# Kernel optimization log

Measured on AMD Instinct MI355X. Metric: run time of the kernel, lower is better.

The kernel has to match this reference:

```python
import jax, jax.numpy as jnp
import numpy as np

N = 8192        # batch rows
D = 1024        # final_dim (power of 2, == init_dim so padding = 0)
STACK = 4       # nbr_stack
SIGMA = 1.0


def _hadamard(n):
    H = np.array([[1.0]], dtype=np.float32)
    while H.shape[0] < n:
        H = np.block([[H, H], [H, -H]])
    return H


def setup_inputs() -> dict:
    key = jax.random.key(0)
    x = jax.random.normal(key, (N, D), dtype=jnp.float32)
    rs = np.random.RandomState(0)
    # B: random signs (diag), shape (STACK, D)
    B = jnp.asarray(rs.choice([-1.0, 1.0], size=(STACK, D)).astype(np.float32))
    # G: gaussian diag, flattened to (STACK*D,)
    G2 = rs.randn(STACK, D).astype(np.float32)
    G = jnp.asarray(G2.reshape(STACK * D))
    # S: chi-like scaling normalized by per-stack norm of G, flattened
    G_norm = np.linalg.norm(G2, axis=1, keepdims=True)
    S2 = (np.abs(rs.randn(STACK, D)).astype(np.float32) * np.sqrt(D)) / G_norm
    S = jnp.asarray(S2.reshape(STACK * D).astype(np.float32))
    # H: dense Walsh-Hadamard matrix (D, D), +-1 entries (non-trainable constant)
    H = jnp.asarray(_hadamard(D))
    # P: per-stack permutation with stack offsets, gathered along feature axis
    P = jnp.asarray(np.concatenate([rs.permutation(D) + i * D for i in range(STACK)]).astype(np.int32))
    bias = jnp.zeros((2 * STACK * D,), dtype=jnp.float32)
    return {"x": x, "B": B, "G": G, "S": S, "bias": bias, "H": H, "P": P}


def reference(x, B, G, S, bias, H, P):
    n = x.shape[0]
    # padding = final_dim - init_dim = 0 here; pad kept for faithfulness
    xp = jnp.pad(x.reshape(-1, D), ((0, 0), (0, 0)))
    # diag B then Hadamard matmul: [n, STACK, D]
    h = xp[:, None, :] * B
    h = jnp.einsum('nsd,de->nse', h, H).reshape(n, STACK * D)
    # permutation gather, diag G
    h = h[:, P] * G
    # second Hadamard matmul
    h = jnp.einsum('nsd,de->nse', h.reshape(n, STACK, D), H).reshape(n, STACK * D)
    # scale by 1/(sigma*sqrt(D)) and diag S
    h = (1.0 / (SIGMA * np.sqrt(D))) * h * S
    # cos/sin random-feature activation
    out = np.sqrt(1.0 / D).astype(np.float32) * jnp.concatenate([jnp.cos(h), jnp.sin(h)], axis=1)
    out = out + bias
    return out
```

## Files before the change

### kernel.cpp

```cpp
#include <hip/hip_runtime.h>


#define FF_D 1024
#define FF_STACK 4
#define FF_NT 256

#define SWZF(vf, OFF) \
    __int_as_float(__builtin_amdgcn_ds_swizzle(__float_as_int(vf), (OFF)))

#define STAGE_BIT(vv, m) { \
    _Pragma("unroll") \
    for (int i_ = 0; i_ < 16; ++i_) \
        if (!(i_ & (m))) { \
            float s_ = vv[i_] + vv[i_ | (m)]; \
            float d_ = vv[i_] - vv[i_ | (m)]; \
            vv[i_] = s_; vv[i_ | (m)] = d_; \
        } \
}

#define STAGE_SWZ(vv, OFF, sgn) { \
    float p_[16]; \
    _Pragma("unroll") \
    for (int i_ = 0; i_ < 16; ++i_) p_[i_] = SWZF(vv[i_], OFF); \
    _Pragma("unroll") \
    for (int i_ = 0; i_ < 16; ++i_) vv[i_] = __builtin_fmaf(sgn, vv[i_], p_[i_]); \
}

#define STAGE_X32(vv, sgn) { \
    float p_[16]; \
    _Pragma("unroll") \
    for (int i_ = 0; i_ < 16; ++i_) p_[i_] = __shfl_xor(vv[i_], 32, 64); \
    _Pragma("unroll") \
    for (int i_ = 0; i_ < 16; ++i_) vv[i_] = __builtin_fmaf(sgn, vv[i_], p_[i_]); \
}

#define FWHT10(vv) { \
    STAGE_BIT(vv, 1) STAGE_BIT(vv, 2) STAGE_BIT(vv, 4) STAGE_BIT(vv, 8) \
    STAGE_SWZ(vv, 0x041F, sg1)   \
    STAGE_SWZ(vv, 0x081F, sg2)   \
    STAGE_SWZ(vv, 0x101F, sg4)   \
    STAGE_SWZ(vv, 0x201F, sg8)   \
    STAGE_SWZ(vv, 0x401F, sg16)  \
    STAGE_X32(vv, sg32)          \
}

__global__ __launch_bounds__(FF_NT) void fastfood_kernel(
    const float* __restrict__ x,
    const float* __restrict__ Bs,
    const float* __restrict__ G,
    const float* __restrict__ S,
    const float* __restrict__ bias,
    const int*   __restrict__ P,
    float* __restrict__ out)
{
    __shared__ float lds[FF_STACK * FF_D];
    const int lane = threadIdx.x & 63;
    const int s    = threadIdx.x >> 6;
    const int row  = blockIdx.x;
    const int sb   = s << 10;
    float* wl = lds + sb;

    const float sg1  = (lane & 1)  ? -1.0f : 1.0f;
    const float sg2  = (lane & 2)  ? -1.0f : 1.0f;
    const float sg4  = (lane & 4)  ? -1.0f : 1.0f;
    const float sg8  = (lane & 8)  ? -1.0f : 1.0f;
    const float sg16 = (lane & 16) ? -1.0f : 1.0f;
    const float sg32 = (lane & 32) ? -1.0f : 1.0f;

    const float kout = 0.03125f;
    const float karg = 0.03125f * 0.15915494309f;

    float v[16];

    #pragma unroll
    for (int q = 0; q < 4; ++q) {
        const float4 t  = *(const float4*)&x[((long long)row << 10) + (q << 8) + (lane << 2)];
        const float4 b4 = *(const float4*)&Bs[sb + (q << 8) + (lane << 2)];
        v[4*q+0] = t.x * b4.x; v[4*q+1] = t.y * b4.y;
        v[4*q+2] = t.z * b4.z; v[4*q+3] = t.w * b4.w;
    }

    FWHT10(v)

    #pragma unroll
    for (int q = 0; q < 4; ++q)
        *(float4*)&wl[(q << 8) | (lane << 2)] =
            make_float4(v[4*q], v[4*q+1], v[4*q+2], v[4*q+3]);
    __builtin_amdgcn_wave_barrier();
    #pragma unroll
    for (int q = 0; q < 4; ++q) {
        const int jb = sb + (q << 8) + (lane << 2);
        const int4   p4 = *(const int4*)&P[jb];
        const float4 g4 = *(const float4*)&G[jb];
        v[4*q+0] = wl[p4.x & (FF_D - 1)] * g4.x;
        v[4*q+1] = wl[p4.y & (FF_D - 1)] * g4.y;
        v[4*q+2] = wl[p4.z & (FF_D - 1)] * g4.z;
        v[4*q+3] = wl[p4.w & (FF_D - 1)] * g4.w;
    }

    FWHT10(v)

    const long long obase = ((long long)row << 13);
    #pragma unroll
    for (int q = 0; q < 4; ++q) {
        const int j = sb + (q << 8) + (lane << 2);
        const float4 s4  = *(const float4*)&S[j];
        const float4 bc4 = *(const float4*)&bias[j];
        const float4 bs4 = *(const float4*)&bias[FF_STACK * FF_D + j];
        float4 oc, os;
        {
            const float tr = __builtin_amdgcn_fractf(v[4*q+0] * (s4.x * karg));
            oc.x = __builtin_amdgcn_cosf(tr) * kout + bc4.x;
            os.x = __builtin_amdgcn_sinf(tr) * kout + bs4.x;
        }
        {
            const float tr = __builtin_amdgcn_fractf(v[4*q+1] * (s4.y * karg));
            oc.y = __builtin_amdgcn_cosf(tr) * kout + bc4.y;
            os.y = __builtin_amdgcn_sinf(tr) * kout + bs4.y;
        }
        {
            const float tr = __builtin_amdgcn_fractf(v[4*q+2] * (s4.z * karg));
            oc.z = __builtin_amdgcn_cosf(tr) * kout + bc4.z;
            os.z = __builtin_amdgcn_sinf(tr) * kout + bs4.z;
        }
        {
            const float tr = __builtin_amdgcn_fractf(v[4*q+3] * (s4.w * karg));
            oc.w = __builtin_amdgcn_cosf(tr) * kout + bc4.w;
            os.w = __builtin_amdgcn_sinf(tr) * kout + bs4.w;
        }
        *(float4*)&out[obase + j] = oc;
        *(float4*)&out[obase + FF_STACK * FF_D + j] = os;
    }
}

extern "C" void kernel_launch(void* const* d_in, const int* in_sizes, int n_in,
                              void* d_out, int out_size, void* d_ws, size_t ws_size,
                              hipStream_t stream) {
    const float* x    = (const float*)d_in[0];
    const float* B    = (const float*)d_in[1];
    const float* G    = (const float*)d_in[2];
    const float* S    = (const float*)d_in[3];
    const float* bias = (const float*)d_in[4];
    const int*   P    = (const int*)d_in[6];
    float* out = (float*)d_out;

    const int n_rows = in_sizes[0] / FF_D;
    fastfood_kernel<<<n_rows, FF_NT, 0, stream>>>(x, B, G, S, bias, P, out);
}
```

Measured before the change: 326.3 us.

## Process two rows per block to reuse B, P, G, S, bias loads and add ILP

Each block now handles two consecutive rows, interleaving both FWHT pipelines so swizzles and butterflies of two independent rows overlap. The per-stack constants (B, P, G, S, bias) are loaded once and shared by both rows, and the P/G loads are hoisted ahead of the LDS write. The cost is twice the register and LDS footprint per block and half as many blocks, which may lower occupancy. It assumes an even row count.

```diff
diff --git a/kernel.cpp b/kernel.cpp
--- a/kernel.cpp
+++ b/kernel.cpp
@@ -8,40 +8,58 @@
 #define SWZF(vf, OFF) \
     __int_as_float(__builtin_amdgcn_ds_swizzle(__float_as_int(vf), (OFF)))
 
-#define STAGE_BIT(vv, m) { \
+#define STAGE_BIT2(aa, bb, m) { \
     _Pragma("unroll") \
     for (int i_ = 0; i_ < 16; ++i_) \
         if (!(i_ & (m))) { \
-            float s_ = vv[i_] + vv[i_ | (m)]; \
-            float d_ = vv[i_] - vv[i_ | (m)]; \
-            vv[i_] = s_; vv[i_ | (m)] = d_; \
+            float sa_ = aa[i_] + aa[i_ | (m)]; \
+            float da_ = aa[i_] - aa[i_ | (m)]; \
+            aa[i_] = sa_; aa[i_ | (m)] = da_; \
+            float sb_ = bb[i_] + bb[i_ | (m)]; \
+            float db_ = bb[i_] - bb[i_ | (m)]; \
+            bb[i_] = sb_; bb[i_ | (m)] = db_; \
         } \
 }
 
-#define STAGE_SWZ(vv, OFF, sgn) { \
-    float p_[16]; \
+#define STAGE_SWZ2(aa, bb, OFF, sgn) { \
+    float pa_[16], pb_[16]; \
     _Pragma("unroll") \
-    for (int i_ = 0; i_ < 16; ++i_) p_[i_] = SWZF(vv[i_], OFF); \
+    for (int i_ = 0; i_ < 16; ++i_) pa_[i_] = SWZF(aa[i_], OFF); \
     _Pragma("unroll") \
-    for (int i_ = 0; i_ < 16; ++i_) vv[i_] = __builtin_fmaf(sgn, vv[i_], p_[i_]); \
+    for (int i_ = 0; i_ < 16; ++i_) pb_[i_] = SWZF(bb[i_], OFF); \
+    _Pragma("unroll") \
+    for (int i_ = 0; i_ < 16; ++i_) aa[i_] = __builtin_fmaf(sgn, aa[i_], pa_[i_]); \
+    _Pragma("unroll") \
+    for (int i_ = 0; i_ < 16; ++i_) bb[i_] = __builtin_fmaf(sgn, bb[i_], pb_[i_]); \
 }
 
-#define STAGE_X32(vv, sgn) { \
-    float p_[16]; \
+#define STAGE_X32_2(aa, bb, sgn) { \
+    float pa_[16], pb_[16]; \
     _Pragma("unroll") \
-    for (int i_ = 0; i_ < 16; ++i_) p_[i_] = __shfl_xor(vv[i_], 32, 64); \
+    for (int i_ = 0; i_ < 16; ++i_) pa_[i_] = __shfl_xor(aa[i_], 32, 64); \
     _Pragma("unroll") \
-    for (int i_ = 0; i_ < 16; ++i_) vv[i_] = __builtin_fmaf(sgn, vv[i_], p_[i_]); \
+    for (int i_ = 0; i_ < 16; ++i_) pb_[i_] = __shfl_xor(bb[i_], 32, 64); \
+    _Pragma("unroll") \
+    for (int i_ = 0; i_ < 16; ++i_) aa[i_] = __builtin_fmaf(sgn, aa[i_], pa_[i_]); \
+    _Pragma("unroll") \
+    for (int i_ = 0; i_ < 16; ++i_) bb[i_] = __builtin_fmaf(sgn, bb[i_], pb_[i_]); \
 }
 
-#define FWHT10(vv) { \
-    STAGE_BIT(vv, 1) STAGE_BIT(vv, 2) STAGE_BIT(vv, 4) STAGE_BIT(vv, 8) \
-    STAGE_SWZ(vv, 0x041F, sg1)   \
-    STAGE_SWZ(vv, 0x081F, sg2)   \
-    STAGE_SWZ(vv, 0x101F, sg4)   \
-    STAGE_SWZ(vv, 0x201F, sg8)   \
-    STAGE_SWZ(vv, 0x401F, sg16)  \
-    STAGE_X32(vv, sg32)          \
+#define FWHT10_2(aa, bb) { \
+    STAGE_BIT2(aa, bb, 1) STAGE_BIT2(aa, bb, 2) \
+    STAGE_BIT2(aa, bb, 4) STAGE_BIT2(aa, bb, 8) \
+    STAGE_SWZ2(aa, bb, 0x041F, sg1)   \
+    STAGE_SWZ2(aa, bb, 0x081F, sg2)   \
+    STAGE_SWZ2(aa, bb, 0x101F, sg4)   \
+    STAGE_SWZ2(aa, bb, 0x201F, sg8)   \
+    STAGE_SWZ2(aa, bb, 0x401F, sg16)  \
+    STAGE_X32_2(aa, bb, sg32)         \
+}
+
+#define CS1(val, sc, bc, bs, oC, oS) { \
+    const float tr_ = __builtin_amdgcn_fractf((val) * ((sc) * karg)); \
+    oC = __builtin_amdgcn_cosf(tr_) * kout + (bc); \
+    oS = __builtin_amdgcn_sinf(tr_) * kout + (bs); \
 }
 
 __global__ __launch_bounds__(FF_NT) void fastfood_kernel(
@@ -53,12 +71,13 @@
     const int*   __restrict__ P,
     float* __restrict__ out)
 {
-    __shared__ float lds[FF_STACK * FF_D];
+    __shared__ float lds[2 * FF_STACK * FF_D];
     const int lane = threadIdx.x & 63;
     const int s    = threadIdx.x >> 6;
-    const int row  = blockIdx.x;
+    const int row0 = blockIdx.x << 1;
     const int sb   = s << 10;
-    float* wl = lds + sb;
+    float* wl0 = lds + sb;
+    float* wl1 = lds + FF_STACK * FF_D + sb;
 
     const float sg1  = (lane & 1)  ? -1.0f : 1.0f;
     const float sg2  = (lane & 2)  ? -1.0f : 1.0f;
@@ -70,66 +89,73 @@
     const float kout = 0.03125f;
     const float karg = 0.03125f * 0.15915494309f;
 
-    float v[16];
+    float v0[16], v1[16];
 
+    const long long xb0 = ((long long)row0 << 10);
     #pragma unroll
     for (int q = 0; q < 4; ++q) {
-        const float4 t  = *(const float4*)&x[((long long)row << 10) + (q << 8) + (lane << 2)];
-        const float4 b4 = *(const float4*)&Bs[sb + (q << 8) + (lane << 2)];
-        v[4*q+0] = t.x * b4.x; v[4*q+1] = t.y * b4.y;
-        v[4*q+2] = t.z * b4.z; v[4*q+3] = t.w * b4.w;
+        const int eo = (q << 8) + (lane << 2);
+        const float4 t0 = *(const float4*)&x[xb0 + eo];
+        const float4 t1 = *(const float4*)&x[xb0 + FF_D + eo];
+        const float4 b4 = *(const float4*)&Bs[sb + eo];
+        v0[4*q+0] = t0.x * b4.x; v0[4*q+1] = t0.y * b4.y;
+        v0[4*q+2] = t0.z * b4.z; v0[4*q+3] = t0.w * b4.w;
+        v1[4*q+0] = t1.x * b4.x; v1[4*q+1] = t1.y * b4.y;
+        v1[4*q+2] = t1.z * b4.z; v1[4*q+3] = t1.w * b4.w;
     }
 
-    FWHT10(v)
+    FWHT10_2(v0, v1)
 
+    int4   p4[4];
+    float4 g4[4];
     #pragma unroll
-    for (int q = 0; q < 4; ++q)
-        *(float4*)&wl[(q << 8) | (lane << 2)] =
-            make_float4(v[4*q], v[4*q+1], v[4*q+2], v[4*q+3]);
+    for (int q = 0; q < 4; ++q) {
+        const int jb = sb + (q << 8) + (lane << 2);
+        p4[q] = *(const int4*)&P[jb];
+        g4[q] = *(const float4*)&G[jb];
+    }
+    #pragma unroll
+    for (int q = 0; q < 4; ++q) {
+        const int eo = (q << 8) | (lane << 2);
+        *(float4*)&wl0[eo] = make_float4(v0[4*q], v0[4*q+1], v0[4*q+2], v0[4*q+3]);
+        *(float4*)&wl1[eo] = make_float4(v1[4*q], v1[4*q+1], v1[4*q+2], v1[4*q+3]);
+    }
     __builtin_amdgcn_wave_barrier();
     #pragma unroll
     for (int q = 0; q < 4; ++q) {
-        const int jb = sb + (q << 8) + (lane << 2);
-        const int4   p4 = *(const int4*)&P[jb];
-        const float4 g4 = *(const float4*)&G[jb];
-        v[4*q+0] = wl[p4.x & (FF_D - 1)] * g4.x;
-        v[4*q+1] = wl[p4.y & (FF_D - 1)] * g4.y;
-        v[4*q+2] = wl[p4.z & (FF_D - 1)] * g4.z;
-        v[4*q+3] = wl[p4.w & (FF_D - 1)] * g4.w;
+        const int ix = p4[q].x & (FF_D - 1);
+        const int iy = p4[q].y & (FF_D - 1);
+        const int iz = p4[q].z & (FF_D - 1);
+        const int iw = p4[q].w & (FF_D - 1);
+        v0[4*q+0] = wl0[ix] * g4[q].x;  v1[4*q+0] = wl1[ix] * g4[q].x;
+        v0[4*q+1] = wl0[iy] * g4[q].y;  v1[4*q+1] = wl1[iy] * g4[q].y;
+        v0[4*q+2] = wl0[iz] * g4[q].z;  v1[4*q+2] = wl1[iz] * g4[q].z;
+        v0[4*q+3] = wl0[iw] * g4[q].w;  v1[4*q+3] = wl1[iw] * g4[q].w;
     }
 
-    FWHT10(v)
+    FWHT10_2(v0, v1)
 
-    const long long obase = ((long long)row << 13);
+    const long long ob0 = ((long long)row0 << 13);
+    const long long ob1 = ob0 + (FF_STACK * FF_D * 2);
     #pragma unroll
     for (int q = 0; q < 4; ++q) {
         const int j = sb + (q << 8) + (lane << 2);
         const float4 s4  = *(const float4*)&S[j];
         const float4 bc4 = *(const float4*)&bias[j];
         const float4 bs4 = *(const float4*)&bias[FF_STACK * FF_D + j];
-        float4 oc, os;
-        {
-            const float tr = __builtin_amdgcn_fractf(v[4*q+0] * (s4.x * karg));
-            oc.x = __builtin_amdgcn_cosf(tr) * kout + bc4.x;
-            os.x = __builtin_amdgcn_sinf(tr) * kout + bs4.x;
-        }
-        {
-            const float tr = __builtin_amdgcn_fractf(v[4*q+1] * (s4.y * karg));
-            oc.y = __builtin_amdgcn_cosf(tr) * kout + bc4.y;
-            os.y = __builtin_amdgcn_sinf(tr) * kout + bs4.y;
-        }
-        {
-            const float tr = __builtin_amdgcn_fractf(v[4*q+2] * (s4.z * karg));
-            oc.z = __builtin_amdgcn_cosf(tr) * kout + bc4.z;
-            os.z = __builtin_amdgcn_sinf(tr) * kout + bs4.z;
-        }
-        {
-            const float tr = __builtin_amdgcn_fractf(v[4*q+3] * (s4.w * karg));
-            oc.w = __builtin_amdgcn_cosf(tr) * kout + bc4.w;
-            os.w = __builtin_amdgcn_sinf(tr) * kout + bs4.w;
-        }
-        *(float4*)&out[obase + j] = oc;
-        *(float4*)&out[obase + FF_STACK * FF_D + j] = os;
+        float4 oc0, os0, oc1, os1;
+        CS1(v0[4*q+0], s4.x, bc4.x, bs4.x, oc0.x, os0.x)
+        CS1(v1[4*q+0], s4.x, bc4.x, bs4.x, oc1.x, os1.x)
+        CS1(v0[4*q+1], s4.y, bc4.y, bs4.y, oc0.y, os0.y)
+        CS1(v1[4*q+1], s4.y, bc4.y, bs4.y, oc1.y, os1.y)
+        CS1(v0[4*q+2], s4.z, bc4.z, bs4.z, oc0.z, os0.z)
+        CS1(v1[4*q+2], s4.z, bc4.z, bs4.z, oc1.z, os1.z)
+        CS1(v0[4*q+3], s4.w, bc4.w, bs4.w, oc0.w, os0.w)
+        CS1(v1[4*q+3], s4.w, bc4.w, bs4.w, oc1.w, os1.w)
+        *(float4*)&out[ob0 + j] = oc0;
+        *(float4*)&out[ob0 + FF_STACK * FF_D + j] = os0;
+        *(float4*)&out[ob1 + j] = oc1;
+        *(float4*)&out[ob1 + FF_STACK * FF_D + j] = os1;
     }
 }
 
@@ -145,5 +171,5 @@
     float* out = (float*)d_out;
 
     const int n_rows = in_sizes[0] / FF_D;
-    fastfood_kernel<<<n_rows, FF_NT, 0, stream>>>(x, B, G, S, bias, P, out);
+    fastfood_kernel<<<n_rows / 2, FF_NT, 0, stream>>>(x, B, G, S, bias, P, out);
 }
```

Result: faster. 305.3 us (-6.4%).

## Split each Hadamard stack across two waves and use DPP for lane butterflies

Applied to the files above, without the earlier changes.

Each 1024-point transform is now split across two waves, with each thread holding 8 values instead of 16. The top butterfly stage is folded into the loads by combining own and partner halves of the input, so each wave reads both halves. The grid doubles to two blocks per row. Several ds_swizzle lane exchanges are replaced with DPP quad_perm and row_ror moves, and launch_bounds asks for 6 blocks per CU. The aim is lower register pressure and more parallelism. The cost is twice the global loads of x, B, P and G, plus a block-wide __syncthreads in place of the wave barrier.

```diff
diff --git a/kernel.cpp b/kernel.cpp
--- a/kernel.cpp
+++ b/kernel.cpp
@@ -8,9 +8,13 @@
 #define SWZF(vf, OFF) \
     __int_as_float(__builtin_amdgcn_ds_swizzle(__float_as_int(vf), (OFF)))
 
-#define STAGE_BIT(vv, m) { \
+#define DPPF(vf, CTRL) \
+    __int_as_float(__builtin_amdgcn_update_dpp( \
+        __float_as_int(vf), __float_as_int(vf), (CTRL), 0xF, 0xF, false))
+
+#define STAGE_BIT8(vv, m) { \
     _Pragma("unroll") \
-    for (int i_ = 0; i_ < 16; ++i_) \
+    for (int i_ = 0; i_ < 8; ++i_) \
         if (!(i_ & (m))) { \
             float s_ = vv[i_] + vv[i_ | (m)]; \
             float d_ = vv[i_] - vv[i_ | (m)]; \
@@ -18,33 +22,47 @@
         } \
 }
 
-#define STAGE_SWZ(vv, OFF, sgn) { \
-    float p_[16]; \
+#define STAGE_DPP8(vv, CTRL, sgn) { \
+    float p_[8]; \
     _Pragma("unroll") \
-    for (int i_ = 0; i_ < 16; ++i_) p_[i_] = SWZF(vv[i_], OFF); \
+    for (int i_ = 0; i_ < 8; ++i_) p_[i_] = DPPF(vv[i_], CTRL); \
     _Pragma("unroll") \
-    for (int i_ = 0; i_ < 16; ++i_) vv[i_] = __builtin_fmaf(sgn, vv[i_], p_[i_]); \
+    for (int i_ = 0; i_ < 8; ++i_) vv[i_] = __builtin_fmaf(sgn, vv[i_], p_[i_]); \
 }
 
-#define STAGE_X32(vv, sgn) { \
-    float p_[16]; \
+#define STAGE_SWZ8(vv, OFF, sgn) { \
+    float p_[8]; \
     _Pragma("unroll") \
-    for (int i_ = 0; i_ < 16; ++i_) p_[i_] = __shfl_xor(vv[i_], 32, 64); \
+    for (int i_ = 0; i_ < 8; ++i_) p_[i_] = SWZF(vv[i_], OFF); \
     _Pragma("unroll") \
-    for (int i_ = 0; i_ < 16; ++i_) vv[i_] = __builtin_fmaf(sgn, vv[i_], p_[i_]); \
+    for (int i_ = 0; i_ < 8; ++i_) vv[i_] = __builtin_fmaf(sgn, vv[i_], p_[i_]); \
 }
 
-#define FWHT10(vv) { \
-    STAGE_BIT(vv, 1) STAGE_BIT(vv, 2) STAGE_BIT(vv, 4) STAGE_BIT(vv, 8) \
-    STAGE_SWZ(vv, 0x041F, sg1)   \
-    STAGE_SWZ(vv, 0x081F, sg2)   \
-    STAGE_SWZ(vv, 0x101F, sg4)   \
-    STAGE_SWZ(vv, 0x201F, sg8)   \
-    STAGE_SWZ(vv, 0x401F, sg16)  \
-    STAGE_X32(vv, sg32)          \
+#define STAGE_X32_8(vv, sgn) { \
+    float p_[8]; \
+    _Pragma("unroll") \
+    for (int i_ = 0; i_ < 8; ++i_) p_[i_] = __shfl_xor(vv[i_], 32, 64); \
+    _Pragma("unroll") \
+    for (int i_ = 0; i_ < 8; ++i_) vv[i_] = __builtin_fmaf(sgn, vv[i_], p_[i_]); \
 }
 
-__global__ __launch_bounds__(FF_NT) void fastfood_kernel(
+#define FWHT9(vv) { \
+    STAGE_BIT8(vv, 1) STAGE_BIT8(vv, 2) STAGE_BIT8(vv, 4) \
+    STAGE_DPP8(vv, 0xB1, sgL1)     \
+    STAGE_DPP8(vv, 0x4E, sgL2)     \
+    STAGE_SWZ8(vv, 0x101F, sgL4)   \
+    STAGE_DPP8(vv, 0x128, sgL8)    \
+    STAGE_SWZ8(vv, 0x401F, sgL16)  \
+    STAGE_X32_8(vv, sgL32)         \
+}
+
+#define CS1(val, sc, bc, bs, oC, oS) { \
+    const float tr_ = __builtin_amdgcn_fractf((val) * ((sc) * karg)); \
+    oC = __builtin_amdgcn_cosf(tr_) * kout + (bc); \
+    oS = __builtin_amdgcn_sinf(tr_) * kout + (bs); \
+}
+
+__global__ __launch_bounds__(FF_NT, 6) void fastfood_kernel(
     const float* __restrict__ x,
     const float* __restrict__ Bs,
     const float* __restrict__ G,
@@ -53,83 +71,93 @@
     const int*   __restrict__ P,
     float* __restrict__ out)
 {
-    __shared__ float lds[FF_STACK * FF_D];
-    const int lane = threadIdx.x & 63;
-    const int s    = threadIdx.x >> 6;
-    const int row  = blockIdx.x;
+    __shared__ float park[2][FF_D];
+    const int tid  = threadIdx.x;
+    const int lane = tid & 63;
+    const int wave = tid >> 6;
+    const int w    = wave & 1;
+    const int sl   = wave >> 1;
+    const int row  = blockIdx.x >> 1;
+    const int s    = ((blockIdx.x & 1) << 1) | sl;
     const int sb   = s << 10;
-    float* wl = lds + sb;
 
-    const float sg1  = (lane & 1)  ? -1.0f : 1.0f;
-    const float sg2  = (lane & 2)  ? -1.0f : 1.0f;
-    const float sg4  = (lane & 4)  ? -1.0f : 1.0f;
-    const float sg8  = (lane & 8)  ? -1.0f : 1.0f;
-    const float sg16 = (lane & 16) ? -1.0f : 1.0f;
-    const float sg32 = (lane & 32) ? -1.0f : 1.0f;
+    const float sgW   = w          ? -1.0f : 1.0f;
+    const float sgL1  = (lane & 1)  ? -1.0f : 1.0f;
+    const float sgL2  = (lane & 2)  ? -1.0f : 1.0f;
+    const float sgL4  = (lane & 4)  ? -1.0f : 1.0f;
+    const float sgL8  = (lane & 8)  ? -1.0f : 1.0f;
+    const float sgL16 = (lane & 16) ? -1.0f : 1.0f;
+    const float sgL32 = (lane & 32) ? -1.0f : 1.0f;
 
     const float kout = 0.03125f;
     const float karg = 0.03125f * 0.15915494309f;
 
-    float v[16];
+    float v[8];
+
+    const long long xb = (long long)row << 10;
+    #pragma unroll
+    for (int q = 0; q < 2; ++q) {
+        const int own = (w << 9) | (q << 8) | (lane << 2);
+        const int par = own ^ 512;
+        const float4 xo = *(const float4*)&x[xb + own];
+        const float4 xp = *(const float4*)&x[xb + par];
+        const float4 bo = *(const float4*)&Bs[sb + own];
+        const float4 bp = *(const float4*)&Bs[sb + par];
+        v[4*q+0] = __builtin_fmaf(sgW, bo.x * xo.x, bp.x * xp.x);
+        v[4*q+1] = __builtin_fmaf(sgW, bo.y * xo.y, bp.y * xp.y);
+        v[4*q+2] = __builtin_fmaf(sgW, bo.z * xo.z, bp.z * xp.z);
+        v[4*q+3] = __builtin_fmaf(sgW, bo.w * xo.w, bp.w * xp.w);
+    }
+
+    FWHT9(v)
+
+    int4   po[2], pp[2];
+    float4 go[2], gp[2];
+    #pragma unroll
+    for (int q = 0; q < 2; ++q) {
+        const int own = (w << 9) | (q << 8) | (lane << 2);
+        const int par = own ^ 512;
+        po[q] = *(const int4*)&P[sb + own];
+        pp[q] = *(const int4*)&P[sb + par];
+        go[q] = *(const float4*)&G[sb + own];
+        gp[q] = *(const float4*)&G[sb + par];
+    }
 
     #pragma unroll
-    for (int q = 0; q < 4; ++q) {
-        const float4 t  = *(const float4*)&x[((long long)row << 10) + (q << 8) + (lane << 2)];
-        const float4 b4 = *(const float4*)&Bs[sb + (q << 8) + (lane << 2)];
-        v[4*q+0] = t.x * b4.x; v[4*q+1] = t.y * b4.y;
-        v[4*q+2] = t.z * b4.z; v[4*q+3] = t.w * b4.w;
+    for (int q = 0; q < 2; ++q) {
+        const int own = (w << 9) | (q << 8) | (lane << 2);
+        *(float4*)&park[sl][own] = make_float4(v[4*q], v[4*q+1], v[4*q+2], v[4*q+3]);
+    }
+    __syncthreads();
+
+    #pragma unroll
+    for (int q = 0; q < 2; ++q) {
+        v[4*q+0] = __builtin_fmaf(sgW, park[sl][po[q].x & (FF_D-1)] * go[q].x,
+                                       park[sl][pp[q].x & (FF_D-1)] * gp[q].x);
+        v[4*q+1] = __builtin_fmaf(sgW, park[sl][po[q].y & (FF_D-1)] * go[q].y,
+                                       park[sl][pp[q].y & (FF_D-1)] * gp[q].y);
+        v[4*q+2] = __builtin_fmaf(sgW, park[sl][po[q].z & (FF_D-1)] * go[q].z,
+                                       park[sl][pp[q].z & (FF_D-1)] * gp[q].z);
+        v[4*q+3] = __builtin_fmaf(sgW, park[sl][po[q].w & (FF_D-1)] * go[q].w,
+                                       park[sl][pp[q].w & (FF_D-1)] * gp[q].w);
     }
 
-    FWHT10(v)
+    FWHT9(v)
 
+    const long long ob = (long long)row << 13;
     #pragma unroll
-    for (int q = 0; q < 4; ++q)
-        *(float4*)&wl[(q << 8) | (lane << 2)] =
-            make_float4(v[4*q], v[4*q+1], v[4*q+2], v[4*q+3]);
-    __builtin_amdgcn_wave_barrier();
-    #pragma unroll
-    for (int q = 0; q < 4; ++q) {
-        const int jb = sb + (q << 8) + (lane << 2);
-        const int4   p4 = *(const int4*)&P[jb];
-        const float4 g4 = *(const float4*)&G[jb];
-        v[4*q+0] = wl[p4.x & (FF_D - 1)] * g4.x;
-        v[4*q+1] = wl[p4.y & (FF_D - 1)] * g4.y;
-        v[4*q+2] = wl[p4.z & (FF_D - 1)] * g4.z;
-        v[4*q+3] = wl[p4.w & (FF_D - 1)] * g4.w;
-    }
-
-    FWHT10(v)
-
-    const long long obase = ((long long)row << 13);
-    #pragma unroll
-    for (int q = 0; q < 4; ++q) {
-        const int j = sb + (q << 8) + (lane << 2);
+    for (int q = 0; q < 2; ++q) {
+        const int j = sb + ((w << 9) | (q << 8) | (lane << 2));
         const float4 s4  = *(const float4*)&S[j];
         const float4 bc4 = *(const float4*)&bias[j];
         const float4 bs4 = *(const float4*)&bias[FF_STACK * FF_D + j];
         float4 oc, os;
-        {
-            const float tr = __builtin_amdgcn_fractf(v[4*q+0] * (s4.x * karg));
-            oc.x = __builtin_amdgcn_cosf(tr) * kout + bc4.x;
-            os.x = __builtin_amdgcn_sinf(tr) * kout + bs4.x;
-        }
-        {
-            const float tr = __builtin_amdgcn_fractf(v[4*q+1] * (s4.y * karg));
-            oc.y = __builtin_amdgcn_cosf(tr) * kout + bc4.y;
-            os.y = __builtin_amdgcn_sinf(tr) * kout + bs4.y;
-        }
-        {
-            const float tr = __builtin_amdgcn_fractf(v[4*q+2] * (s4.z * karg));
-            oc.z = __builtin_amdgcn_cosf(tr) * kout + bc4.z;
-            os.z = __builtin_amdgcn_sinf(tr) * kout + bs4.z;
-        }
-        {
-            const float tr = __builtin_amdgcn_fractf(v[4*q+3] * (s4.w * karg));
-            oc.w = __builtin_amdgcn_cosf(tr) * kout + bc4.w;
-            os.w = __builtin_amdgcn_sinf(tr) * kout + bs4.w;
-        }
-        *(float4*)&out[obase + j] = oc;
-        *(float4*)&out[obase + FF_STACK * FF_D + j] = os;
+        CS1(v[4*q+0], s4.x, bc4.x, bs4.x, oc.x, os.x)
+        CS1(v[4*q+1], s4.y, bc4.y, bs4.y, oc.y, os.y)
+        CS1(v[4*q+2], s4.z, bc4.z, bs4.z, oc.z, os.z)
+        CS1(v[4*q+3], s4.w, bc4.w, bs4.w, oc.w, os.w)
+        *(float4*)&out[ob + j] = oc;
+        *(float4*)&out[ob + FF_STACK * FF_D + j] = os;
     }
 }
 
@@ -145,5 +173,5 @@
     float* out = (float*)d_out;
 
     const int n_rows = in_sizes[0] / FF_D;
-    fastfood_kernel<<<n_rows, FF_NT, 0, stream>>>(x, B, G, S, bias, P, out);
+    fastfood_kernel<<<n_rows * 2, FF_NT, 0, stream>>>(x, B, G, S, bias, P, out);
 }
```

Result: slower. 341.4 us (+4.6%).
